# Performance work log

Measured on AMD Instinct MI355X. Metric: run time of the kernel, lower is better.

## Reference

```python
import jax, jax.numpy as jnp
import numpy as np

B, T, D, U = 64, 2048, 1024, 1024

def setup_inputs() -> dict:
    key = jax.random.key(0)
    k1, k2, k3 = jax.random.split(key, 3)
    inputs = jax.random.normal(k1, (B, T, D), dtype=jnp.float32)
    W_x = jax.random.normal(k2, (D, U), dtype=jnp.float32) * (1.0 / np.sqrt(D))
    W_h = jax.random.normal(k3, (U, U), dtype=jnp.float32) * (1.0 / np.sqrt(U))
    b = jnp.zeros((U,), dtype=jnp.float32)
    return {"inputs": inputs, "W_x": W_x, "W_h": W_h, "b": b}

def reference(inputs, W_x, W_h, b):
    # Elman RNN: h_t = tanh(x_t @ W_x + h_{t-1} @ W_h + b); return final h.
    # Precompute input projections for all timesteps in one big GEMM.
    xp = jnp.einsum('btd,du->btu', inputs, W_x) + b  # [B, T, U]
    h0 = jnp.zeros((inputs.shape[0], W_h.shape[0]), dtype=inputs.dtype)

    def step(h, x_t):
        h = jnp.tanh(x_t + h @ W_h)
        return h, None

    h_final, _ = jax.lax.scan(step, h0, jnp.swapaxes(xp, 0, 1))  # scan over time
    return h_final
```

## Files before the change

kernel.cpp:

```cpp
#include <hip/hip_runtime.h>
#include <stdint.h>

#define NB 64
#define NT 2048
#define ND 1024
#define NU 1024
#define RETRY_MAX (1 << 20)

typedef __attribute__((ext_vector_type(8))) short bf16x8;
typedef __attribute__((ext_vector_type(4))) float f32x4;
typedef unsigned long long u64;

__device__ __forceinline__ unsigned short f2bf(float f) {
  union { float f; unsigned u; } v; v.f = f;
  return (unsigned short)((v.u + 0x7FFFu + ((v.u >> 16) & 1u)) >> 16);
}

__global__ void init_ws(unsigned* __restrict__ ws) {
  const int n = 1024 + 2 * NB * NU;
  for (int i = blockIdx.x * blockDim.x + threadIdx.x; i < n; i += gridDim.x * blockDim.x)
    ws[i] = (i < 4) ? 0xFFFFFFFFu : 0u;
}

__launch_bounds__(256, 3)
__global__ void gemm_xp(const float* __restrict__ inp, const float* __restrict__ Wx,
                        const float* __restrict__ bias, float* __restrict__ xp,
                        int t0, int Tc) {
  __shared__ unsigned short As[128][56];
  __shared__ unsigned short Bs[128][56];

  const int tid = threadIdx.x;
  const int u0 = blockIdx.x * 128;
  const int m_base = blockIdx.y * 128;
  const int b = m_base / Tc;
  const int tc0 = m_base % Tc;
  const size_t arow0 = ((size_t)b * NT + t0 + tc0) * (size_t)ND;

  const int w = tid >> 6, lane = tid & 63;
  const int wr = w >> 1, wc = w & 1;
  const int l15 = lane & 15, lk = lane >> 4;
  const int srow = tid & 127;
  const int shalf = tid >> 7;

  f32x4 acc[4][4];
  #pragma unroll
  for (int i = 0; i < 4; ++i)
    #pragma unroll
    for (int j = 0; j < 4; ++j)
      acc[i][j] = (f32x4){0.f, 0.f, 0.f, 0.f};

  for (int k0 = 0; k0 < ND; k0 += 32) {
    __syncthreads();
    {
      const float* src = inp + arow0 + (size_t)srow * ND + k0 + shalf * 16;
      unsigned short tmp[16];
      #pragma unroll
      for (int i = 0; i < 16; i += 4) {
        float4 v = *(const float4*)(src + i);
        tmp[i + 0] = f2bf(v.x); tmp[i + 1] = f2bf(v.y);
        tmp[i + 2] = f2bf(v.z); tmp[i + 3] = f2bf(v.w);
      }
      #pragma unroll
      for (int h = 0; h < 2; ++h) {
        bf16x8 pv;
        #pragma unroll
        for (int j = 0; j < 8; ++j) pv[j] = (short)tmp[h * 8 + j];
        *(bf16x8*)&As[srow][shalf * 16 + h * 8] = pv;
      }
    }
    {
      const float* src = Wx + (size_t)(k0 + shalf * 16) * NU + u0 + srow;
      unsigned short tmp[16];
      #pragma unroll
      for (int i = 0; i < 16; ++i) tmp[i] = f2bf(src[(size_t)i * NU]);
      #pragma unroll
      for (int h = 0; h < 2; ++h) {
        bf16x8 pv;
        #pragma unroll
        for (int j = 0; j < 8; ++j) pv[j] = (short)tmp[h * 8 + j];
        *(bf16x8*)&Bs[srow][shalf * 16 + h * 8] = pv;
      }
    }
    __syncthreads();

    bf16x8 af[4], bfr[4];
    #pragma unroll
    for (int mf = 0; mf < 4; ++mf)
      af[mf] = *(const bf16x8*)&As[wr * 64 + mf * 16 + l15][lk * 8];
    #pragma unroll
    for (int nf = 0; nf < 4; ++nf)
      bfr[nf] = *(const bf16x8*)&Bs[wc * 64 + nf * 16 + l15][lk * 8];
    #pragma unroll
    for (int mf = 0; mf < 4; ++mf)
      #pragma unroll
      for (int nf = 0; nf < 4; ++nf)
        acc[mf][nf] = __builtin_amdgcn_mfma_f32_16x16x32_bf16(af[mf], bfr[nf], acc[mf][nf], 0, 0, 0);
  }

  #pragma unroll
  for (int nf = 0; nf < 4; ++nf) {
    const int col = u0 + wc * 64 + nf * 16 + l15;
    const float bv = bias[col];
    #pragma unroll
    for (int mf = 0; mf < 4; ++mf) {
      const int rbase = m_base + wr * 64 + mf * 16 + lk * 4;
      #pragma unroll
      for (int r = 0; r < 4; ++r)
        xp[(size_t)(rbase + r) * NU + col] = acc[mf][nf][r] + bv;
    }
  }
}

__launch_bounds__(512, 1)
__global__ void scan_kernel(const float* __restrict__ Wh, const float* __restrict__ xp,
                            unsigned* __restrict__ hw, float* __restrict__ out,
                            unsigned* __restrict__ ws, int t0, int Tc, int chunk) {
  __shared__ float Red[8][64][20];
  __shared__ unsigned s_slot, s_tk;

  const int tid = threadIdx.x;
  unsigned xcc;
  asm volatile("s_getreg_b32 %0, hwreg(HW_REG_XCC_ID)" : "=s"(xcc));

  unsigned* slots   = ws;
  unsigned* tickets = ws + 16;

  if (tid == 0) {
    unsigned slot = 0xFFFFFFFFu;
    #pragma unroll
    for (int s = 0; s < 4; ++s) {
      unsigned exp = 0xFFFFFFFFu;
      __hip_atomic_compare_exchange_strong(&slots[s], &exp, xcc,
          __ATOMIC_RELAXED, __ATOMIC_RELAXED, __HIP_MEMORY_SCOPE_AGENT);
      const unsigned v = __hip_atomic_load(&slots[s], __ATOMIC_RELAXED, __HIP_MEMORY_SCOPE_AGENT);
      if (v == xcc) { slot = (unsigned)s; break; }
    }
    unsigned tk = 0xFFFFu;
    if (slot <= 3u)
      tk = __hip_atomic_fetch_add(&tickets[slot * 16 + chunk], 1u,
                                  __ATOMIC_RELAXED, __HIP_MEMORY_SCOPE_AGENT);
    s_slot = slot; s_tk = tk;
  }
  __syncthreads();
  if (s_slot > 3u || s_tk >= 16u) return;
  const int cluster = (int)s_slot;
  const int j = (int)s_tk;

  const int r0 = cluster * 16;
  const int gc0 = j * 64;
  const int lane = tid & 63;
  const int k8 = tid >> 6;
  const int l15 = lane & 15;
  const int lk = lane >> 4;

  bf16x8 Bf[4][4];
  for (int nf = 0; nf < 4; ++nf)
    for (int kq = 0; kq < 4; ++kq) {
      const int col = gc0 + nf * 16 + l15;
      bf16x8 v;
      #pragma unroll
      for (int jj = 0; jj < 8; ++jj) {
        const int k = k8 * 128 + kq * 32 + lk * 8 + jj;
        v[jj] = (short)f2bf(Wh[(size_t)k * NU + col]);
      }
      Bf[nf][kq] = v;
    }

  const int rcol = tid & 63;
  const int rq = tid >> 6;
  const int gcol = gc0 + rcol;
  const bool reducer = tid < 256;

  for (int tc = 0; tc < Tc; ++tc) {
    const int t = t0 + tc;
    const unsigned* hc = hw + (size_t)(t & 1) * (NB * NU);
    unsigned* hn = hw + (size_t)((t + 1) & 1) * (NB * NU);
    const unsigned tagn = ((unsigned)(t + 1)) << 16;

    float xpv[4];
    if (reducer) {
      #pragma unroll
      for (int r = 0; r < 4; ++r)
        xpv[r] = xp[((size_t)(r0 + rq * 4 + r) * Tc + tc) * NU + gcol];
    }

    f32x4 acc[4];
    #pragma unroll
    for (int nf = 0; nf < 4; ++nf) acc[nf] = (f32x4){0.f, 0.f, 0.f, 0.f};

    if (t != 0) {
      u64 wv[16];
      const unsigned* pb = hc + (size_t)(r0 + l15) * NU + k8 * 128 + lk * 8;
      const unsigned tgt = (unsigned)t;
      for (int it = 0; it < RETRY_MAX; ++it) {
        #pragma unroll
        for (int kq = 0; kq < 4; ++kq)
          #pragma unroll
          for (int q = 0; q < 4; ++q)
            wv[kq * 4 + q] = __hip_atomic_load((const u64*)(pb + kq * 32 + q * 2),
                                               __ATOMIC_RELAXED, __HIP_MEMORY_SCOPE_AGENT);
        bool ok = true;
        #pragma unroll
        for (int i = 0; i < 16; ++i)
          ok &= (((unsigned)wv[i]) >> 16) >= tgt;
        if (__all(ok)) break;
        __builtin_amdgcn_s_sleep(1);
      }

      #pragma unroll
      for (int kq = 0; kq < 4; ++kq) {
        union { unsigned u[4]; bf16x8 v; } a;
        #pragma unroll
        for (int q = 0; q < 4; ++q) {
          const u64 w2 = wv[kq * 4 + q];
          a.u[q] = ((unsigned)w2 & 0xffffu) | (((unsigned)(w2 >> 32)) << 16);
        }
        #pragma unroll
        for (int nf = 0; nf < 4; ++nf)
          acc[nf] = __builtin_amdgcn_mfma_f32_16x16x32_bf16(a.v, Bf[nf][kq], acc[nf], 0, 0, 0);
      }
    }

    #pragma unroll
    for (int nf = 0; nf < 4; ++nf)
      *(f32x4*)&Red[k8][nf * 16 + l15][lk * 4] = acc[nf];
    __syncthreads();

    if (reducer) {
      f32x4 s = *(const f32x4*)&Red[0][rcol][rq * 4];
      #pragma unroll
      for (int q = 1; q < 8; ++q)
        s += *(const f32x4*)&Red[q][rcol][rq * 4];
      #pragma unroll
      for (int r = 0; r < 4; ++r) {
        const int row = rq * 4 + r;
        const float z = s[r] + xpv[r];
        const float e = __expf(2.0f * z);
        const float hv = 1.0f - 2.0f / (e + 1.0f);
        if (t == NT - 1) out[(size_t)(r0 + row) * NU + gcol] = hv;
        const unsigned word = tagn | (unsigned)f2bf(hv);
        const unsigned pw = (unsigned)__shfl_xor((int)word, 1);
        if (!(lane & 1)) {
          const u64 dw = (u64)word | ((u64)pw << 32);
          __hip_atomic_store((u64*)(hn + (size_t)(r0 + row) * NU + gcol), dw,
                             __ATOMIC_RELAXED, __HIP_MEMORY_SCOPE_AGENT);
        }
      }
    }
    __syncthreads();
  }
}

extern "C" void kernel_launch(void* const* d_in, const int* in_sizes, int n_in,
                              void* d_out, int out_size, void* d_ws, size_t ws_size,
                              hipStream_t stream) {
  (void)in_sizes; (void)n_in; (void)out_size;
  const float* inp  = (const float*)d_in[0];
  const float* Wx   = (const float*)d_in[1];
  const float* Wh   = (const float*)d_in[2];
  const float* bias = (const float*)d_in[3];
  float* out = (float*)d_out;

  unsigned* ws = (unsigned*)d_ws;
  unsigned* hw = (unsigned*)((char*)d_ws + 4096);
  const size_t xp_off = 4096 + (size_t)2 * NB * NU * sizeof(unsigned);
  float* xp = (float*)((char*)d_ws + xp_off);
  const size_t avail = (ws_size > xp_off) ? ws_size - xp_off : 0;

  int Tc = 128;
  for (int cand = NT; cand >= 128; cand >>= 1)
    if ((size_t)NB * (size_t)cand * NU * sizeof(float) <= avail) { Tc = cand; break; }

  init_ws<<<dim3(128), dim3(256), 0, stream>>>(ws);

  for (int t0 = 0; t0 < NT; t0 += Tc) {
    gemm_xp<<<dim3(8, (NB * Tc) / 128), dim3(256), 0, stream>>>(inp, Wx, bias, xp, t0, Tc);
    scan_kernel<<<dim3(256), dim3(512), 0, stream>>>(Wh, xp, hw, out, ws, t0, Tc, t0 / Tc);
  }
}
```

Baseline: 13.13 ms.

## Add per-XCD L2 fast-path polling with duplicated hidden state buffer

```diff
diff --git a/kernel.cpp b/kernel.cpp
--- a/kernel.cpp
+++ b/kernel.cpp
@@ -6,9 +6,11 @@
 #define ND 1024
 #define NU 1024
 #define RETRY_MAX (1 << 20)
+#define NFAST 32
 
 typedef __attribute__((ext_vector_type(8))) short bf16x8;
 typedef __attribute__((ext_vector_type(4))) float f32x4;
+typedef __attribute__((ext_vector_type(2))) unsigned u32x2;
 typedef unsigned long long u64;
 
 __device__ __forceinline__ unsigned short f2bf(float f) {
@@ -16,8 +18,14 @@
   return (unsigned short)((v.u + 0x7FFFu + ((v.u >> 16) & 1u)) >> 16);
 }
 
+__device__ __forceinline__ u32x2 load_x2_sc0(const unsigned* p) {
+  u32x2 r;
+  asm volatile("global_load_dwordx2 %0, %1, off sc0" : "=&v"(r) : "v"(p));
+  return r;
+}
+
 __global__ void init_ws(unsigned* __restrict__ ws) {
-  const int n = 1024 + 2 * NB * NU;
+  const int n = 1024 + 4 * NB * NU;
   for (int i = blockIdx.x * blockDim.x + threadIdx.x; i < n; i += gridDim.x * blockDim.x)
     ws[i] = (i < 4) ? 0xFFFFFFFFu : 0u;
 }
@@ -113,7 +121,8 @@
 
 __launch_bounds__(512, 1)
 __global__ void scan_kernel(const float* __restrict__ Wh, const float* __restrict__ xp,
-                            unsigned* __restrict__ hw, float* __restrict__ out,
+                            unsigned* __restrict__ hw, unsigned* __restrict__ hl3,
+                            float* __restrict__ out,
                             unsigned* __restrict__ ws, int t0, int Tc, int chunk) {
   __shared__ float Red[8][64][20];
   __shared__ unsigned s_slot, s_tk;
@@ -173,8 +182,8 @@
 
   for (int tc = 0; tc < Tc; ++tc) {
     const int t = t0 + tc;
-    const unsigned* hc = hw + (size_t)(t & 1) * (NB * NU);
-    unsigned* hn = hw + (size_t)((t + 1) & 1) * (NB * NU);
+    const size_t cur = (size_t)(t & 1) * (NB * NU);
+    const size_t nxt = (size_t)((t + 1) & 1) * (NB * NU);
     const unsigned tagn = ((unsigned)(t + 1)) << 16;
 
     float xpv[4];
@@ -189,32 +198,63 @@
     for (int nf = 0; nf < 4; ++nf) acc[nf] = (f32x4){0.f, 0.f, 0.f, 0.f};
 
     if (t != 0) {
-      u64 wv[16];
-      const unsigned* pb = hc + (size_t)(r0 + l15) * NU + k8 * 128 + lk * 8;
       const unsigned tgt = (unsigned)t;
-      for (int it = 0; it < RETRY_MAX; ++it) {
+      const size_t boff = (size_t)(r0 + l15) * NU + k8 * 128 + lk * 8;
+      unsigned pk[16];
+      bool got = false;
+
+      const unsigned* pbL2 = hw + cur + boff;
+      for (int it = 0; it < NFAST; ++it) {
+        asm volatile("buffer_inv sc1" ::: "memory");
+        u32x2 fv[16];
         #pragma unroll
         for (int kq = 0; kq < 4; ++kq)
           #pragma unroll
           for (int q = 0; q < 4; ++q)
-            wv[kq * 4 + q] = __hip_atomic_load((const u64*)(pb + kq * 32 + q * 2),
-                                               __ATOMIC_RELAXED, __HIP_MEMORY_SCOPE_AGENT);
-        bool ok = true;
-        #pragma unroll
-        for (int i = 0; i < 16; ++i)
-          ok &= (((unsigned)wv[i]) >> 16) >= tgt;
-        if (__all(ok)) break;
+            fv[kq * 4 + q] = load_x2_sc0(pbL2 + kq * 32 + q * 2);
+        asm volatile("s_waitcnt vmcnt(0)" ::: "memory");
+        __builtin_amdgcn_sched_barrier(0);
+        unsigned d = 0;
+        #pragma unroll
+        for (int i = 0; i < 16; ++i) d |= (fv[i].x >> 16) ^ tgt;
+        if (__all(d == 0)) {
+          #pragma unroll
+          for (int i = 0; i < 16; ++i) pk[i] = (fv[i].x & 0xffffu) | (fv[i].y << 16);
+          got = true;
+          break;
+        }
         __builtin_amdgcn_s_sleep(1);
+      }
+
+      if (!got) {
+        const unsigned* pbL3 = hl3 + cur + boff;
+        u64 wv[16];
+        for (int it = 0; it < RETRY_MAX; ++it) {
+          #pragma unroll
+          for (int kq = 0; kq < 4; ++kq)
+            #pragma unroll
+            for (int q = 0; q < 4; ++q)
+              wv[kq * 4 + q] = __hip_atomic_load((const u64*)(pbL3 + kq * 32 + q * 2),
+                                                 __ATOMIC_RELAXED, __HIP_MEMORY_SCOPE_AGENT);
+          bool ok = true;
+          #pragma unroll
+          for (int i = 0; i < 16; ++i)
+            ok &= (((unsigned)wv[i]) >> 16) >= tgt;
+          if (__all(ok)) break;
+          __builtin_amdgcn_s_sleep(1);
+        }
+        #pragma unroll
+        for (int i = 0; i < 16; ++i) {
+          const unsigned lo = (unsigned)wv[i], hi = (unsigned)(wv[i] >> 32);
+          pk[i] = (lo & 0xffffu) | (hi << 16);
+        }
       }
 
       #pragma unroll
       for (int kq = 0; kq < 4; ++kq) {
         union { unsigned u[4]; bf16x8 v; } a;
         #pragma unroll
-        for (int q = 0; q < 4; ++q) {
-          const u64 w2 = wv[kq * 4 + q];
-          a.u[q] = ((unsigned)w2 & 0xffffu) | (((unsigned)(w2 >> 32)) << 16);
-        }
+        for (int q = 0; q < 4; ++q) a.u[q] = pk[kq * 4 + q];
         #pragma unroll
         for (int nf = 0; nf < 4; ++nf)
           acc[nf] = __builtin_amdgcn_mfma_f32_16x16x32_bf16(a.v, Bf[nf][kq], acc[nf], 0, 0, 0);
@@ -242,7 +282,10 @@
         const unsigned pw = (unsigned)__shfl_xor((int)word, 1);
         if (!(lane & 1)) {
           const u64 dw = (u64)word | ((u64)pw << 32);
-          __hip_atomic_store((u64*)(hn + (size_t)(r0 + row) * NU + gcol), dw,
+          const size_t off = nxt + (size_t)(r0 + row) * NU + gcol;
+          __hip_atomic_store((u64*)(hw + off), dw,
+                             __ATOMIC_RELAXED, __HIP_MEMORY_SCOPE_WORKGROUP);
+          __hip_atomic_store((u64*)(hl3 + off), dw,
                              __ATOMIC_RELAXED, __HIP_MEMORY_SCOPE_AGENT);
         }
       }
@@ -261,9 +304,10 @@
   const float* bias = (const float*)d_in[3];
   float* out = (float*)d_out;
 
-  unsigned* ws = (unsigned*)d_ws;
-  unsigned* hw = (unsigned*)((char*)d_ws + 4096);
-  const size_t xp_off = 4096 + (size_t)2 * NB * NU * sizeof(unsigned);
+  unsigned* ws  = (unsigned*)d_ws;
+  unsigned* hw  = (unsigned*)((char*)d_ws + 4096);
+  unsigned* hl3 = hw + 2 * NB * NU;
+  const size_t xp_off = 4096 + (size_t)4 * NB * NU * sizeof(unsigned);
   float* xp = (float*)((char*)d_ws + xp_off);
   const size_t avail = (ws_size > xp_off) ? ws_size - xp_off : 0;
 
@@ -275,6 +319,6 @@
 
   for (int t0 = 0; t0 < NT; t0 += Tc) {
     gemm_xp<<<dim3(8, (NB * Tc) / 128), dim3(256), 0, stream>>>(inp, Wx, bias, xp, t0, Tc);
-    scan_kernel<<<dim3(256), dim3(512), 0, stream>>>(Wh, xp, hw, out, ws, t0, Tc, t0 / Tc);
-  }
-}
+    scan_kernel<<<dim3(256), dim3(512), 0, stream>>>(Wh, xp, hw, hl3, out, ws, t0, Tc, t0 / Tc);
+  }
+}
```

Result: slower. 22.41 ms, median of 2 (+70.7%).
